# Kernel optimization log

Measured on AMD Instinct MI355X. Metric: run time of the kernel, lower is better.

The kernel has to match this reference:

```python
import jax, jax.numpy as jnp
import numpy as np
import math

IN_DIM = 256
OUT_DIM = 256
MAX_IN = 1024
MAX_OUT = 512
BATCH = 2
SEQ = 1024  # actual_seq_len == max_in_seq here
RED = 2
LN_EPS = 1e-5


def setup_inputs() -> dict:
    key = jax.random.key(0)
    ks = jax.random.split(key, 8)
    N = BATCH * SEQ
    return {
        "x": jax.random.normal(ks[0], (N, IN_DIM), dtype=jnp.float32),
        "M": jax.random.uniform(ks[1], (OUT_DIM, IN_DIM), minval=-0.5, maxval=0.5, dtype=jnp.float32),
        "P": jax.random.uniform(ks[2], (OUT_DIM, OUT_DIM), minval=-0.1, maxval=0.1, dtype=jnp.float32),
        "Linker": jax.random.uniform(ks[3], (MAX_IN, MAX_OUT), minval=-0.1, maxval=0.1, dtype=jnp.float32),
        "ln_gamma": jnp.ones((OUT_DIM,), dtype=jnp.float32),
        "ln_beta": jnp.zeros((OUT_DIM,), dtype=jnp.float32),
        "res_W": jax.random.uniform(ks[4], (OUT_DIM, IN_DIM), minval=-0.1, maxval=0.1, dtype=jnp.float32),
        "res_linker": jax.random.uniform(ks[5], (MAX_IN, MAX_OUT), minval=-0.1, maxval=0.1, dtype=jnp.float32),
        "actual_seq_len": SEQ,
    }


def _layer_norm(z, gamma, beta):
    mu = jnp.mean(z, axis=-1, keepdims=True)
    var = jnp.mean((z - mu) ** 2, axis=-1, keepdims=True)
    return (z - mu) * jax.lax.rsqrt(var + LN_EPS) * gamma + beta


def _periods():
    i = jnp.arange(OUT_DIM, dtype=jnp.float32)[:, None]
    j = jnp.arange(OUT_DIM, dtype=jnp.float32)[None, :]
    return i * OUT_DIM + j + 2.0  # (D, D)


def reference(x, M, P, Linker, ln_gamma, ln_beta, res_W, res_linker, actual_seq_len):
    S = int(actual_seq_len)
    N, _ = x.shape
    B = N // S
    D = OUT_DIM
    out_seq = max(1, S // RED)

    # Z = LN(x @ M^T)
    Z = _layer_norm(x @ M.T, ln_gamma, ln_beta)  # (N, D)

    # position transform: T[k,i] = sum_j Z[k,j] * P[i,j] * cos(2*pi*k / periods[i,j])
    k = jnp.arange(N, dtype=jnp.float32)[:, None, None]  # (N,1,1)
    phi = jnp.cos(2.0 * math.pi * k / _periods()[None])   # (N, D, D)
    T = jnp.einsum('kj,ij,kij->ki', Z, P, phi)            # (N, D)

    # adaptive sequence-length transform via Linker slice
    L = Linker[:S, :out_seq]                               # (S, out_seq)
    U = jnp.einsum('bsd,st->btd', T.reshape(B, S, D), L).reshape(B * out_seq, D)

    # 'separate' residual path
    rfeat = (x @ res_W.T).reshape(B, S, D)
    rL = res_linker[:S, :out_seq]
    residual = jnp.einsum('bsd,st->btd', rfeat, rL).reshape(B * out_seq, D)

    return U + residual
```

## Files before the change

### kernel.cpp

```cpp
#include <hip/hip_runtime.h>

#define D256 256
#define KT 8
#define S_SEQ 1024
#define OUTSEQ 512

typedef __attribute__((ext_vector_type(8))) short bf16x8;
typedef __attribute__((ext_vector_type(8))) unsigned short u16x8;
typedef __attribute__((ext_vector_type(4))) unsigned short u16x4;
typedef __attribute__((ext_vector_type(4))) float f32x4;

__device__ inline unsigned short f2bf(float f) {
  unsigned u = __float_as_uint(f);
  return (unsigned short)((u + 0x7fffu + ((u >> 16) & 1u)) >> 16);
}

__device__ inline bf16x8 ld8bf(const float* p) {
  const float4 v0 = *(const float4*)p;
  const float4 v1 = *(const float4*)(p + 4);
  bf16x8 r;
  r[0] = (short)f2bf(v0.x); r[1] = (short)f2bf(v0.y);
  r[2] = (short)f2bf(v0.z); r[3] = (short)f2bf(v0.w);
  r[4] = (short)f2bf(v1.x); r[5] = (short)f2bf(v1.y);
  r[6] = (short)f2bf(v1.z); r[7] = (short)f2bf(v1.w);
  return r;
}

__global__ __launch_bounds__(256) void k_pre(const float* __restrict__ x,
                                             const float* __restrict__ M,
                                             const float* __restrict__ resW,
                                             const float* __restrict__ P,
                                             const float* __restrict__ Linker,
                                             const float* __restrict__ rLinker,
                                             const float* __restrict__ gamma,
                                             const float* __restrict__ beta,
                                             float4* __restrict__ PIt4,
                                             unsigned short* __restrict__ LinkTb,
                                             float* __restrict__ Zb,
                                             unsigned short* __restrict__ Bt) {
  __shared__ float smem[8224];
  const int tid = threadIdx.x;
  const int blk = blockIdx.x;

  if (blk < 128) {
    float (*Zs)[D256] = (float(*)[D256])smem;
    float (*Rs)[D256] = (float(*)[D256])(smem + 4096);
    float* mu_s = smem + 8192;
    float* rs_s = smem + 8208;
    const int k0 = blk * 16;
    const int w = tid >> 6;
    const int l = tid & 63;
    const int m = l & 15, q = l >> 4;

    f32x4 aZ[4] = {}, aR[4] = {};
    const float* xrow = x + (size_t)(k0 + m) * D256;
    #pragma unroll
    for (int ks = 0; ks < 8; ++ks) {
      const bf16x8 a = ld8bf(xrow + ks * 32 + q * 8);
      #pragma unroll
      for (int cf = 0; cf < 4; ++cf) {
        const int o = w * 64 + cf * 16 + m;
        const bf16x8 bz = ld8bf(M    + (size_t)o * D256 + ks * 32 + q * 8);
        const bf16x8 br = ld8bf(resW + (size_t)o * D256 + ks * 32 + q * 8);
        aZ[cf] = __builtin_amdgcn_mfma_f32_16x16x32_bf16(a, bz, aZ[cf], 0, 0, 0);
        aR[cf] = __builtin_amdgcn_mfma_f32_16x16x32_bf16(a, br, aR[cf], 0, 0, 0);
      }
    }
    #pragma unroll
    for (int cf = 0; cf < 4; ++cf) {
      #pragma unroll
      for (int r = 0; r < 4; ++r) {
        Zs[q * 4 + r][w * 64 + cf * 16 + m] = aZ[cf][r];
        Rs[q * 4 + r][w * 64 + cf * 16 + m] = aR[cf][r];
      }
    }
    __syncthreads();

    #pragma unroll
    for (int rr = w; rr < 16; rr += 4) {
      float s = 0.f, sq = 0.f;
      #pragma unroll
      for (int p = 0; p < 4; ++p) {
        const float v = Zs[rr][l + 64 * p];
        s += v;
        sq = fmaf(v, v, sq);
      }
      #pragma unroll
      for (int off = 32; off; off >>= 1) {
        s += __shfl_down(s, off);
        sq += __shfl_down(sq, off);
      }
      if (l == 0) {
        const float mu = s * (1.0f / 256.0f);
        const float var = sq * (1.0f / 256.0f) - mu * mu;
        mu_s[rr] = mu;
        rs_s[rr] = rsqrtf(var + 1e-5f);
      }
    }
    __syncthreads();

    {
      const int t = tid;
      const float g = gamma[t], be = beta[t];
      u16x8 o0, o1;
      #pragma unroll
      for (int rr = 0; rr < 16; ++rr) {
        Zb[(size_t)(k0 + rr) * D256 + t] = (Zs[rr][t] - mu_s[rr]) * rs_s[rr] * g + be;
        const unsigned short rb = f2bf(Rs[rr][t]);
        if (rr < 8) o0[rr] = rb; else o1[rr - 8] = rb;
      }
      unsigned short* dst = Bt + (size_t)t * 4096 + 2048 + k0;
      *(u16x8*)dst = o0;
      *(u16x8*)(dst + 8) = o1;
    }
    return;
  }

  if (blk < 384) {
    const int j = blk - 128;
    const int t = tid;
    const float p = (float)(t * D256 + j + 2);
    const float ip = 1.0f / p;
    const float cb2 = 2.0f * __builtin_amdgcn_cosf(ip);
    PIt4[j * D256 + t] = make_float4(P[t * D256 + j], ip, cb2, 0.0f);
    return;
  }

  float (*tl)[65] = (float(*)[65])smem;
  const int tb = blk - 384;
  const int st = tb & 31;
  const int tt = tb >> 5;
  const int s0 = st * 64, t0 = tt * 64;
  const float* src = (s0 < 1024) ? (Linker + (size_t)s0 * OUTSEQ)
                                 : (rLinker + (size_t)(s0 - 1024) * OUTSEQ);
  {
    const int sy = tid >> 2, sx = tid & 3;
    #pragma unroll
    for (int c = 0; c < 4; ++c) {
      const int ci = sx + c * 4;
      const float4 v = *(const float4*)&src[sy * OUTSEQ + t0 + ci * 4];
      tl[ci * 4 + 0][sy] = v.x;
      tl[ci * 4 + 1][sy] = v.y;
      tl[ci * 4 + 2][sy] = v.z;
      tl[ci * 4 + 3][sy] = v.w;
    }
  }
  __syncthreads();
  {
    const int ty = tid >> 2, tx = tid & 3;
    u16x8 o0, o1;
    #pragma unroll
    for (int e = 0; e < 8; ++e) o0[e] = f2bf(tl[ty][tx * 16 + e]);
    #pragma unroll
    for (int e = 0; e < 8; ++e) o1[e] = f2bf(tl[ty][tx * 16 + 8 + e]);
    unsigned short* dst = LinkTb + (size_t)(t0 + ty) * 2048 + s0 + tx * 16;
    *(u16x8*)dst = o0;
    *(u16x8*)(dst + 8) = o1;
  }
}

__global__ __launch_bounds__(256, 6) void k_B(const float* __restrict__ Zb,
                                              const float4* __restrict__ PIt4,
                                              unsigned short* __restrict__ Bt) {
  __shared__ float buf[5120];
  const int tid = threadIdx.x;
  const int il = tid & 7;
  const int jg = tid >> 3;
  const int ig = blockIdx.x & 31;
  const int kt = blockIdx.x >> 5;
  const int i0 = ig * 8;
  const int k0 = kt * 16;
  const int i  = i0 + il;

  #pragma unroll
  for (int r = 0; r < 16; ++r)
    buf[tid * 20 + r] = Zb[(size_t)(k0 + r) * D256 + tid];
  __syncthreads();

  float acc[16] = {};
  const float kf0 = (float)k0;
  const float4* pip = PIt4 + i;
  #pragma unroll
  for (int jj = 0; jj < 8; ++jj) {
    const int j = jg + 32 * jj;
    const float4 pi = pip[(size_t)j * D256];
    const float4 z0 = *(const float4*)&buf[j * 20 + 0];
    const float4 z1 = *(const float4*)&buf[j * 20 + 4];
    const float4 z2 = *(const float4*)&buf[j * 20 + 8];
    const float4 z3 = *(const float4*)&buf[j * 20 + 12];
    const float a = kf0 * pi.y;
    float c0 = __builtin_amdgcn_cosf(__builtin_amdgcn_fractf(a)) * pi.x;
    float c1 = __builtin_amdgcn_cosf(__builtin_amdgcn_fractf(a + pi.y)) * pi.x;
    acc[0] = fmaf(z0.x, c0, acc[0]);
    acc[1] = fmaf(z0.y, c1, acc[1]);
    float c2;
    c2 = fmaf(pi.z, c1, -c0); acc[2]  = fmaf(z0.z, c2, acc[2]);  c0 = c1; c1 = c2;
    c2 = fmaf(pi.z, c1, -c0); acc[3]  = fmaf(z0.w, c2, acc[3]);  c0 = c1; c1 = c2;
    c2 = fmaf(pi.z, c1, -c0); acc[4]  = fmaf(z1.x, c2, acc[4]);  c0 = c1; c1 = c2;
    c2 = fmaf(pi.z, c1, -c0); acc[5]  = fmaf(z1.y, c2, acc[5]);  c0 = c1; c1 = c2;
    c2 = fmaf(pi.z, c1, -c0); acc[6]  = fmaf(z1.z, c2, acc[6]);  c0 = c1; c1 = c2;
    c2 = fmaf(pi.z, c1, -c0); acc[7]  = fmaf(z1.w, c2, acc[7]);  c0 = c1; c1 = c2;
    c2 = fmaf(pi.z, c1, -c0); acc[8]  = fmaf(z2.x, c2, acc[8]);  c0 = c1; c1 = c2;
    c2 = fmaf(pi.z, c1, -c0); acc[9]  = fmaf(z2.y, c2, acc[9]);  c0 = c1; c1 = c2;
    c2 = fmaf(pi.z, c1, -c0); acc[10] = fmaf(z2.z, c2, acc[10]); c0 = c1; c1 = c2;
    c2 = fmaf(pi.z, c1, -c0); acc[11] = fmaf(z2.w, c2, acc[11]); c0 = c1; c1 = c2;
    c2 = fmaf(pi.z, c1, -c0); acc[12] = fmaf(z3.x, c2, acc[12]); c0 = c1; c1 = c2;
    c2 = fmaf(pi.z, c1, -c0); acc[13] = fmaf(z3.y, c2, acc[13]); c0 = c1; c1 = c2;
    c2 = fmaf(pi.z, c1, -c0); acc[14] = fmaf(z3.z, c2, acc[14]); c0 = c1; c1 = c2;
    c2 = fmaf(pi.z, c1, -c0); acc[15] = fmaf(z3.w, c2, acc[15]);
  }
  __syncthreads();

  #pragma unroll
  for (int k = 0; k < 16; ++k)
    buf[jg * 132 + k * 8 + il] = acc[k];
  __syncthreads();

  float tv = 0.f;
  if (tid < 128) {
    #pragma unroll
    for (int g = 0; g < 32; ++g) tv += buf[g * 132 + tid];
  }
  __syncthreads();
  if (tid < 128) buf[(tid & 7) * 16 + (tid >> 3)] = tv;
  __syncthreads();
  if (tid < 32) {
    const int iw = tid >> 2;
    const int kq = tid & 3;
    const float4 v = *(const float4*)&buf[iw * 16 + kq * 4];
    u16x4 o;
    o[0] = f2bf(v.x); o[1] = f2bf(v.y); o[2] = f2bf(v.z); o[3] = f2bf(v.w);
    *(u16x4*)(Bt + (size_t)(i0 + iw) * 4096 + k0 + kq * 4) = o;
  }
}

__global__ __launch_bounds__(256) void k_Cm(const unsigned short* __restrict__ LinkTb,
                                            const unsigned short* __restrict__ Bt,
                                            float* __restrict__ out) {
  __shared__ float red[4][32][32];
  const int bid = blockIdx.x;
  const int ct = bid & 7;
  const int rt = bid >> 3;
  const int b  = rt >> 4;
  const int t0 = (rt & 15) * 32;
  const int d0 = ct * 32;
  const int w  = threadIdx.x >> 6;
  const int l  = threadIdx.x & 63;
  const int m  = l & 15, q = l >> 4;
  const int s0 = w * 256;

  f32x4 acc00 = {}, acc01 = {}, acc10 = {}, acc11 = {};
  const unsigned short* Arow = LinkTb + (size_t)(t0 + m) * 2048;
  const unsigned short* Brow = Bt + (size_t)(d0 + m) * 4096;

  #pragma unroll
  for (int seg = 0; seg < 2; ++seg) {
    const int acol = seg * 1024 + s0 + q * 8;
    const int bcol = seg * 2048 + b * 1024 + s0 + q * 8;
    #pragma unroll
    for (int ks = 0; ks < 8; ++ks) {
      const bf16x8 a0 = *(const bf16x8*)(Arow + acol + ks * 32);
      const bf16x8 a1 = *(const bf16x8*)(Arow + 16 * 2048 + acol + ks * 32);
      const bf16x8 b0 = *(const bf16x8*)(Brow + bcol + ks * 32);
      const bf16x8 b1 = *(const bf16x8*)(Brow + 16 * 4096 + bcol + ks * 32);
      acc00 = __builtin_amdgcn_mfma_f32_16x16x32_bf16(a0, b0, acc00, 0, 0, 0);
      acc01 = __builtin_amdgcn_mfma_f32_16x16x32_bf16(a0, b1, acc01, 0, 0, 0);
      acc10 = __builtin_amdgcn_mfma_f32_16x16x32_bf16(a1, b0, acc10, 0, 0, 0);
      acc11 = __builtin_amdgcn_mfma_f32_16x16x32_bf16(a1, b1, acc11, 0, 0, 0);
    }
  }

  #pragma unroll
  for (int r = 0; r < 4; ++r) {
    red[w][q * 4 + r][m]           = acc00[r];
    red[w][q * 4 + r][16 + m]      = acc01[r];
    red[w][16 + q * 4 + r][m]      = acc10[r];
    red[w][16 + q * 4 + r][16 + m] = acc11[r];
  }
  __syncthreads();

  const int row = threadIdx.x >> 3;
  const int c4  = (threadIdx.x & 7) * 4;
  const float4 v0 = *(const float4*)&red[0][row][c4];
  const float4 v1 = *(const float4*)&red[1][row][c4];
  const float4 v2 = *(const float4*)&red[2][row][c4];
  const float4 v3 = *(const float4*)&red[3][row][c4];
  float4 s;
  s.x = v0.x + v1.x + v2.x + v3.x;
  s.y = v0.y + v1.y + v2.y + v3.y;
  s.z = v0.z + v1.z + v2.z + v3.z;
  s.w = v0.w + v1.w + v2.w + v3.w;
  *(float4*)&out[(size_t)(b * 512 + t0 + row) * D256 + d0 + c4] = s;
}

extern "C" void kernel_launch(void* const* d_in, const int* in_sizes, int n_in,
                              void* d_out, int out_size, void* d_ws, size_t ws_size,
                              hipStream_t stream) {
  const float* x       = (const float*)d_in[0];
  const float* M       = (const float*)d_in[1];
  const float* P       = (const float*)d_in[2];
  const float* Linker  = (const float*)d_in[3];
  const float* gamma   = (const float*)d_in[4];
  const float* beta    = (const float*)d_in[5];
  const float* resW    = (const float*)d_in[6];
  const float* rLinker = (const float*)d_in[7];
  float* out = (float*)d_out;

  char* ws = (char*)d_ws;
  float4*         PIt4   = (float4*)(ws);
  unsigned short* LinkTb = (unsigned short*)(ws + 1024 * 1024);
  unsigned short* Bt     = (unsigned short*)(ws + 3072 * 1024);
  float*          Zb     = (float*)(ws + 5120 * 1024);

  hipLaunchKernelGGL(k_pre, dim3(640),  dim3(256), 0, stream,
                     x, M, resW, P, Linker, rLinker, gamma, beta,
                     PIt4, LinkTb, Zb, Bt);
  hipLaunchKernelGGL(k_B,   dim3(4096), dim3(256), 0, stream, Zb, PIt4, Bt);
  hipLaunchKernelGGL(k_Cm,  dim3(256),  dim3(256), 0, stream, LinkTb, Bt, out);
}
```

Before: 51.07 us.

## Use stride-2 Chebyshev recurrence with packed FMA and split final GEMM finer

```diff
diff --git a/kernel.cpp b/kernel.cpp
--- a/kernel.cpp
+++ b/kernel.cpp
@@ -1,7 +1,6 @@
 #include <hip/hip_runtime.h>
 
 #define D256 256
-#define KT 8
 #define S_SEQ 1024
 #define OUTSEQ 512
 
@@ -9,6 +8,7 @@
 typedef __attribute__((ext_vector_type(8))) unsigned short u16x8;
 typedef __attribute__((ext_vector_type(4))) unsigned short u16x4;
 typedef __attribute__((ext_vector_type(4))) float f32x4;
+typedef __attribute__((ext_vector_type(2))) float f32x2;
 
 __device__ inline unsigned short f2bf(float f) {
   unsigned u = __float_as_uint(f);
@@ -122,7 +122,8 @@
     const float p = (float)(t * D256 + j + 2);
     const float ip = 1.0f / p;
     const float cb2 = 2.0f * __builtin_amdgcn_cosf(ip);
-    PIt4[j * D256 + t] = make_float4(P[t * D256 + j], ip, cb2, 0.0f);
+    const float D = fmaf(cb2, cb2, -2.0f);
+    PIt4[j * D256 + t] = make_float4(P[t * D256 + j], ip, cb2, D);
     return;
   }
 
@@ -177,43 +178,52 @@
     buf[tid * 20 + r] = Zb[(size_t)(k0 + r) * D256 + tid];
   __syncthreads();
 
-  float acc[16] = {};
+  f32x2 acc[8];
+  #pragma unroll
+  for (int q = 0; q < 8; ++q) acc[q] = (f32x2){0.f, 0.f};
+
   const float kf0 = (float)k0;
-  const float4* pip = PIt4 + i;
+  const f32x4* pip = (const f32x4*)(PIt4 + i);
   #pragma unroll
   for (int jj = 0; jj < 8; ++jj) {
     const int j = jg + 32 * jj;
-    const float4 pi = pip[(size_t)j * D256];
+    const f32x4 pi = pip[(size_t)j * D256];
     const float4 z0 = *(const float4*)&buf[j * 20 + 0];
     const float4 z1 = *(const float4*)&buf[j * 20 + 4];
     const float4 z2 = *(const float4*)&buf[j * 20 + 8];
     const float4 z3 = *(const float4*)&buf[j * 20 + 12];
-    const float a = kf0 * pi.y;
-    float c0 = __builtin_amdgcn_cosf(__builtin_amdgcn_fractf(a)) * pi.x;
-    float c1 = __builtin_amdgcn_cosf(__builtin_amdgcn_fractf(a + pi.y)) * pi.x;
-    acc[0] = fmaf(z0.x, c0, acc[0]);
-    acc[1] = fmaf(z0.y, c1, acc[1]);
-    float c2;
-    c2 = fmaf(pi.z, c1, -c0); acc[2]  = fmaf(z0.z, c2, acc[2]);  c0 = c1; c1 = c2;
-    c2 = fmaf(pi.z, c1, -c0); acc[3]  = fmaf(z0.w, c2, acc[3]);  c0 = c1; c1 = c2;
-    c2 = fmaf(pi.z, c1, -c0); acc[4]  = fmaf(z1.x, c2, acc[4]);  c0 = c1; c1 = c2;
-    c2 = fmaf(pi.z, c1, -c0); acc[5]  = fmaf(z1.y, c2, acc[5]);  c0 = c1; c1 = c2;
-    c2 = fmaf(pi.z, c1, -c0); acc[6]  = fmaf(z1.z, c2, acc[6]);  c0 = c1; c1 = c2;
-    c2 = fmaf(pi.z, c1, -c0); acc[7]  = fmaf(z1.w, c2, acc[7]);  c0 = c1; c1 = c2;
-    c2 = fmaf(pi.z, c1, -c0); acc[8]  = fmaf(z2.x, c2, acc[8]);  c0 = c1; c1 = c2;
-    c2 = fmaf(pi.z, c1, -c0); acc[9]  = fmaf(z2.y, c2, acc[9]);  c0 = c1; c1 = c2;
-    c2 = fmaf(pi.z, c1, -c0); acc[10] = fmaf(z2.z, c2, acc[10]); c0 = c1; c1 = c2;
-    c2 = fmaf(pi.z, c1, -c0); acc[11] = fmaf(z2.w, c2, acc[11]); c0 = c1; c1 = c2;
-    c2 = fmaf(pi.z, c1, -c0); acc[12] = fmaf(z3.x, c2, acc[12]); c0 = c1; c1 = c2;
-    c2 = fmaf(pi.z, c1, -c0); acc[13] = fmaf(z3.y, c2, acc[13]); c0 = c1; c1 = c2;
-    c2 = fmaf(pi.z, c1, -c0); acc[14] = fmaf(z3.z, c2, acc[14]); c0 = c1; c1 = c2;
-    c2 = fmaf(pi.z, c1, -c0); acc[15] = fmaf(z3.w, c2, acc[15]);
-  }
-  __syncthreads();
-
-  #pragma unroll
-  for (int k = 0; k < 16; ++k)
-    buf[jg * 132 + k * 8 + il] = acc[k];
+    const float a  = kf0 * pi.y;
+    const float r0 = __builtin_amdgcn_fractf(a);
+    const float r1 = __builtin_amdgcn_fractf(a + pi.y);
+    const float s0 = __builtin_amdgcn_cosf(r0) * pi.x;
+    const float s1 = __builtin_amdgcn_cosf(r1) * pi.x;
+    const float s2 = fmaf(pi.z, s1, -s0);
+    const float s3 = fmaf(pi.z, s2, -s1);
+    f32x2 P0 = {s0, s1};
+    f32x2 P1 = {s2, s3};
+    const f32x2 D2 = {pi.w, pi.w};
+    acc[0] = __builtin_elementwise_fma((f32x2){z0.x, z0.y}, P0, acc[0]);
+    acc[1] = __builtin_elementwise_fma((f32x2){z0.z, z0.w}, P1, acc[1]);
+    f32x2 Pn;
+#define CSTEP(IDX, ZA, ZB) \
+    Pn = __builtin_elementwise_fma(D2, P1, -P0); \
+    acc[IDX] = __builtin_elementwise_fma((f32x2){ZA, ZB}, Pn, acc[IDX]); \
+    P0 = P1; P1 = Pn;
+    CSTEP(2, z1.x, z1.y)
+    CSTEP(3, z1.z, z1.w)
+    CSTEP(4, z2.x, z2.y)
+    CSTEP(5, z2.z, z2.w)
+    CSTEP(6, z3.x, z3.y)
+    CSTEP(7, z3.z, z3.w)
+#undef CSTEP
+  }
+  __syncthreads();
+
+  #pragma unroll
+  for (int k2 = 0; k2 < 8; ++k2) {
+    buf[jg * 132 + (k2 * 2) * 8 + il]     = acc[k2].x;
+    buf[jg * 132 + (k2 * 2 + 1) * 8 + il] = acc[k2].y;
+  }
   __syncthreads();
 
   float tv = 0.f;
@@ -237,60 +247,45 @@
 __global__ __launch_bounds__(256) void k_Cm(const unsigned short* __restrict__ LinkTb,
                                             const unsigned short* __restrict__ Bt,
                                             float* __restrict__ out) {
-  __shared__ float red[4][32][32];
+  __shared__ float red[4][16][32];
   const int bid = blockIdx.x;
   const int ct = bid & 7;
-  const int rt = bid >> 3;
-  const int b  = rt >> 4;
-  const int t0 = (rt & 15) * 32;
+  const int tt = (bid >> 3) & 31;
+  const int b  = bid >> 8;
+  const int t0 = tt * 16;
   const int d0 = ct * 32;
   const int w  = threadIdx.x >> 6;
   const int l  = threadIdx.x & 63;
   const int m  = l & 15, q = l >> 4;
-  const int s0 = w * 256;
-
-  f32x4 acc00 = {}, acc01 = {}, acc10 = {}, acc11 = {};
-  const unsigned short* Arow = LinkTb + (size_t)(t0 + m) * 2048;
-  const unsigned short* Brow = Bt + (size_t)(d0 + m) * 4096;
-
-  #pragma unroll
-  for (int seg = 0; seg < 2; ++seg) {
-    const int acol = seg * 1024 + s0 + q * 8;
-    const int bcol = seg * 2048 + b * 1024 + s0 + q * 8;
-    #pragma unroll
-    for (int ks = 0; ks < 8; ++ks) {
-      const bf16x8 a0 = *(const bf16x8*)(Arow + acol + ks * 32);
-      const bf16x8 a1 = *(const bf16x8*)(Arow + 16 * 2048 + acol + ks * 32);
-      const bf16x8 b0 = *(const bf16x8*)(Brow + bcol + ks * 32);
-      const bf16x8 b1 = *(const bf16x8*)(Brow + 16 * 4096 + bcol + ks * 32);
-      acc00 = __builtin_amdgcn_mfma_f32_16x16x32_bf16(a0, b0, acc00, 0, 0, 0);
-      acc01 = __builtin_amdgcn_mfma_f32_16x16x32_bf16(a0, b1, acc01, 0, 0, 0);
-      acc10 = __builtin_amdgcn_mfma_f32_16x16x32_bf16(a1, b0, acc10, 0, 0, 0);
-      acc11 = __builtin_amdgcn_mfma_f32_16x16x32_bf16(a1, b1, acc11, 0, 0, 0);
-    }
+  const int seg = w >> 1;
+  const int sh  = w & 1;
+
+  f32x4 acc0 = {}, acc1 = {};
+  const unsigned short* Arow = LinkTb + (size_t)(t0 + m) * 2048 + seg * 1024 + sh * 512 + q * 8;
+  const unsigned short* Brow = Bt + (size_t)(d0 + m) * 4096 + seg * 2048 + b * 1024 + sh * 512 + q * 8;
+
+  #pragma unroll
+  for (int ks = 0; ks < 16; ++ks) {
+    const bf16x8 a0 = *(const bf16x8*)(Arow + ks * 32);
+    const bf16x8 b0 = *(const bf16x8*)(Brow + ks * 32);
+    const bf16x8 b1 = *(const bf16x8*)(Brow + 16 * 4096 + ks * 32);
+    acc0 = __builtin_amdgcn_mfma_f32_16x16x32_bf16(a0, b0, acc0, 0, 0, 0);
+    acc1 = __builtin_amdgcn_mfma_f32_16x16x32_bf16(a0, b1, acc1, 0, 0, 0);
   }
 
   #pragma unroll
   for (int r = 0; r < 4; ++r) {
-    red[w][q * 4 + r][m]           = acc00[r];
-    red[w][q * 4 + r][16 + m]      = acc01[r];
-    red[w][16 + q * 4 + r][m]      = acc10[r];
-    red[w][16 + q * 4 + r][16 + m] = acc11[r];
-  }
-  __syncthreads();
-
-  const int row = threadIdx.x >> 3;
-  const int c4  = (threadIdx.x & 7) * 4;
-  const float4 v0 = *(const float4*)&red[0][row][c4];
-  const float4 v1 = *(const float4*)&red[1][row][c4];
-  const float4 v2 = *(const float4*)&red[2][row][c4];
-  const float4 v3 = *(const float4*)&red[3][row][c4];
-  float4 s;
-  s.x = v0.x + v1.x + v2.x + v3.x;
-  s.y = v0.y + v1.y + v2.y + v3.y;
-  s.z = v0.z + v1.z + v2.z + v3.z;
-  s.w = v0.w + v1.w + v2.w + v3.w;
-  *(float4*)&out[(size_t)(b * 512 + t0 + row) * D256 + d0 + c4] = s;
+    red[w][q * 4 + r][m]      = acc0[r];
+    red[w][q * 4 + r][16 + m] = acc1[r];
+  }
+  __syncthreads();
+
+  const int row = threadIdx.x >> 4;
+  const int c0  = (threadIdx.x & 15) * 2;
+  float2 s;
+  s.x = red[0][row][c0] + red[1][row][c0] + red[2][row][c0] + red[3][row][c0];
+  s.y = red[0][row][c0 + 1] + red[1][row][c0 + 1] + red[2][row][c0 + 1] + red[3][row][c0 + 1];
+  *(float2*)&out[(size_t)(b * 512 + t0 + row) * D256 + d0 + c0] = s;
 }
 
 extern "C" void kernel_launch(void* const* d_in, const int* in_sizes, int n_in,
@@ -316,5 +311,5 @@
                      x, M, resW, P, Linker, rLinker, gamma, beta,
                      PIt4, LinkTb, Zb, Bt);
   hipLaunchKernelGGL(k_B,   dim3(4096), dim3(256), 0, stream, Zb, PIt4, Bt);
-  hipLaunchKernelGGL(k_Cm,  dim3(256),  dim3(256), 0, stream, LinkTb, Bt, out);
-}
+  hipLaunchKernelGGL(k_Cm,  dim3(512),  dim3(256), 0, stream, LinkTb, Bt, out);
+}
```

After: 54.45 us. 6.6% more time.
